# Performance work log

Measured on AMD Instinct MI355X. Metric: run time of the kernel, lower is better.

Reference implementation:

```python
import jax, jax.numpy as jnp
import numpy as np

INF = 1e10  # stand-in for the original global INF constant
D_MODEL = 1024
N_HEADS = 16
SCALE = float(np.sqrt(D_MODEL))  # Attention is built with full d_key, so scale = sqrt(d_model)


def setup_inputs() -> dict:
    key = jax.random.key(0)
    ks = jax.random.split(key, 8)
    B, S, D = 4, 2048, D_MODEL
    s = 1.0 / np.sqrt(D)
    return {
        "query": jax.random.normal(ks[0], (B, S, D), jnp.float32),
        "key": jax.random.normal(ks[1], (B, S, D), jnp.float32),
        "value": jax.random.normal(ks[2], (B, S, D), jnp.float32),
        "wq": jax.random.normal(ks[3], (D, D), jnp.float32) * s,
        "bq": jnp.zeros((D,), jnp.float32),
        "wk": jax.random.normal(ks[4], (D, D), jnp.float32) * s,
        "bk": jnp.zeros((D,), jnp.float32),
        "wv": jax.random.normal(ks[5], (D, D), jnp.float32) * s,
        "bv": jnp.zeros((D,), jnp.float32),
        "wo": jax.random.normal(ks[6], (D, D), jnp.float32) * s,
        "bo": jnp.zeros((D,), jnp.float32),
    }


def reference(query, key, value, wq, bq, wk, bk, wv, bv, wo, bo):
    B, S, D = query.shape
    H = N_HEADS
    dh = D // H
    q = query @ wq + bq
    k = key @ wk + bk
    v = value @ wv + bv
    # split heads: [B, S, H, dh]
    q = q.reshape(B, S, H, dh)
    k = k.reshape(B, S, H, dh)
    v = v.reshape(B, S, H, dh)
    # raw dot products (unscaled), then causal mask subtracted (as in original),
    # then divide by sqrt(d_key) and softmax
    scores = jnp.einsum("bqhd,bkhd->bhqk", q, k)
    causal = jnp.triu(jnp.ones((S, S), scores.dtype), k=1) * INF
    scores = scores - causal  # broadcast over [B, H]
    attn = jax.nn.softmax(scores / SCALE, axis=-1)
    out = jnp.einsum("bhqk,bkhd->bqhd", attn, v).reshape(B, S, D)
    return out @ wo + bo
```

## Files before the change

### kernel.cpp

```cpp
#include <hip/hip_runtime.h>
#include <hip/hip_bf16.h>

typedef __bf16 bf16_t;
typedef __bf16 bf16x8 __attribute__((ext_vector_type(8)));
typedef float f32x4 __attribute__((ext_vector_type(4)));

#define MFMA16(a, b, c) __builtin_amdgcn_mfma_f32_16x16x32_bf16((a), (b), (c), 0, 0, 0)

static constexpr int S_LEN = 2048;
static constexpr int DM = 1024;
static constexpr int NH = 16;
static constexpr int DH = 64;

struct WtArgs { const float* w[4]; bf16_t* o[4]; };

__global__ __launch_bounds__(256) void wt_kernel(WtArgs p) {
    int bid = blockIdx.x;
    int wi = bid >> 8;
    int tb = bid & 255;
    int k0 = (tb >> 4) * 64;
    int n0 = (tb & 15) * 64;
    const float* w = p.w[wi];
    bf16_t* o = p.o[wi];
    __shared__ bf16_t t[64 * 66];
    int tid = threadIdx.x;
#pragma unroll
    for (int i = 0; i < 4; ++i) {
        int f = tid + 256 * i;
        int row = f >> 4;
        int c4 = f & 15;
        f32x4 v = *reinterpret_cast<const f32x4*>(w + (size_t)(k0 + row) * DM + n0 + c4 * 4);
        int base = row * 66 + c4 * 4;
        t[base + 0] = (bf16_t)v[0];
        t[base + 1] = (bf16_t)v[1];
        t[base + 2] = (bf16_t)v[2];
        t[base + 3] = (bf16_t)v[3];
    }
    __syncthreads();
#pragma unroll
    for (int i = 0; i < 2; ++i) {
        int c = tid + 256 * i;
        int n = c >> 3;
        int ck = c & 7;
        union { bf16_t h[8]; uint4 u; } cv;
#pragma unroll
        for (int j = 0; j < 8; ++j) cv.h[j] = t[(ck * 8 + j) * 66 + n];
        *reinterpret_cast<uint4*>(o + (size_t)(n0 + n) * DM + k0 + ck * 8) = cv.u;
    }
}

template <int MODE>
__global__ __launch_bounds__(256) void gemm_k(const void* __restrict__ Ap,
                                              const bf16_t* __restrict__ BT,
                                              const float* __restrict__ bias,
                                              void* __restrict__ Cp, float alpha) {
    constexpr int K = 1024, N = 1024;
    int bid = blockIdx.x;
    int bm = bid >> 3, bn = bid & 7;
    int tid = threadIdx.x;
    int w = tid >> 6, l = tid & 63;
    int g = l >> 4, lc = l & 15;

    __shared__ bf16_t a_lds[128 * 40];
    __shared__ bf16_t b_lds[128 * 40];

    f32x4 zero = {0.f, 0.f, 0.f, 0.f};
    f32x4 acc[4][4];
#pragma unroll
    for (int m = 0; m < 4; ++m)
#pragma unroll
        for (int n = 0; n < 4; ++n) acc[m][n] = zero;

    int m0 = bm * 128, n0 = bn * 128;
    const float* Af = (const float*)Ap;
    const bf16_t* Ab = (const bf16_t*)Ap;
    int wr = (w >> 1) * 64, wc = (w & 1) * 64;

    for (int kt = 0; kt < K / 32; ++kt) {
        int k0 = kt * 32;
        __syncthreads();
        if constexpr (MODE != 1) {
#pragma unroll
            for (int i = 0; i < 4; ++i) {
                int f = tid + 256 * i;
                int row = f >> 3, c4 = f & 7;
                f32x4 v = *reinterpret_cast<const f32x4*>(Af + (size_t)(m0 + row) * K + k0 + c4 * 4);
                union { bf16_t h[4]; uint2 u; } cv;
                cv.h[0] = (bf16_t)v[0]; cv.h[1] = (bf16_t)v[1];
                cv.h[2] = (bf16_t)v[2]; cv.h[3] = (bf16_t)v[3];
                *reinterpret_cast<uint2*>(&a_lds[row * 40 + c4 * 4]) = cv.u;
            }
        } else {
#pragma unroll
            for (int i = 0; i < 2; ++i) {
                int c = tid + 256 * i;
                int row = c >> 2, ch = c & 3;
                uint4 v = *reinterpret_cast<const uint4*>(Ab + (size_t)(m0 + row) * K + k0 + ch * 8);
                *reinterpret_cast<uint4*>(&a_lds[row * 40 + ch * 8]) = v;
            }
        }
#pragma unroll
        for (int i = 0; i < 2; ++i) {
            int c = tid + 256 * i;
            int row = c >> 2, ch = c & 3;
            uint4 v = *reinterpret_cast<const uint4*>(BT + (size_t)(n0 + row) * K + k0 + ch * 8);
            *reinterpret_cast<uint4*>(&b_lds[row * 40 + ch * 8]) = v;
        }
        __syncthreads();

        bf16x8 af[4], bfr[4];
#pragma unroll
        for (int m = 0; m < 4; ++m)
            af[m] = *reinterpret_cast<bf16x8*>(&a_lds[(wr + m * 16 + lc) * 40 + g * 8]);
#pragma unroll
        for (int n = 0; n < 4; ++n)
            bfr[n] = *reinterpret_cast<bf16x8*>(&b_lds[(wc + n * 16 + lc) * 40 + g * 8]);
#pragma unroll
        for (int m = 0; m < 4; ++m)
#pragma unroll
            for (int n = 0; n < 4; ++n)
                acc[m][n] = MFMA16(af[m], bfr[n], acc[m][n]);
    }

#pragma unroll
    for (int n = 0; n < 4; ++n) {
        int ng = n0 + wc + n * 16 + lc;
        float bv = bias[ng];
#pragma unroll
        for (int m = 0; m < 4; ++m) {
#pragma unroll
            for (int r = 0; r < 4; ++r) {
                int mg = m0 + wr + m * 16 + g * 4 + r;
                float v = (acc[m][n][r] + bv) * alpha;
                if constexpr (MODE == 0) {
                    int b = mg >> 11, s = mg & 2047, h = ng >> 6, d = ng & 63;
                    ((bf16_t*)Cp)[(((size_t)(b * NH + h)) * S_LEN + s) * DH + d] = (bf16_t)v;
                } else if constexpr (MODE == 2) {
                    int b = mg >> 11, s = mg & 2047, h = ng >> 6, d = ng & 63;
                    ((bf16_t*)Cp)[(((size_t)(b * NH + h)) * DH + d) * S_LEN + s] = (bf16_t)v;
                } else {
                    ((float*)Cp)[(size_t)mg * N + ng] = v;
                }
            }
        }
    }
}

__global__ __launch_bounds__(256) void attn_kernel(const bf16_t* __restrict__ Qh,
                                                   const bf16_t* __restrict__ Kh,
                                                   const bf16_t* __restrict__ Vt,
                                                   bf16_t* __restrict__ AO) {
    int bid = blockIdx.x;
    int qt = 31 - (bid >> 6);
    int bh = bid & 63;
    int h = bh & 15;
    int b = bh >> 4;
    int tid = threadIdx.x;
    int w = tid >> 6, l = tid & 63;
    int g = l >> 4, lc = l & 15;
    int q0 = qt * 64 + w * 16;
    int q = q0 + lc;

    __shared__ bf16_t k_lds[64 * 80];
    __shared__ bf16_t v_lds[64 * 80];
    __shared__ bf16_t p_lds[4][16 * 80];

    size_t head_off = ((size_t)(b * NH + h)) * S_LEN * DH;
    const bf16_t* Kp = Kh + head_off;
    const bf16_t* Vp = Vt + head_off;

    bf16x8 qf[2];
    {
        const bf16_t* qp = Qh + head_off + (size_t)(q0 + lc) * DH + g * 8;
        qf[0] = *reinterpret_cast<const bf16x8*>(qp);
        qf[1] = *reinterpret_cast<const bf16x8*>(qp + 32);
    }

    f32x4 zero = {0.f, 0.f, 0.f, 0.f};
    f32x4 o_acc[4];
#pragma unroll
    for (int nt = 0; nt < 4; ++nt) o_acc[nt] = zero;
    float m_s = -1e30f, l_s = 0.f;

    int sw = lc & 7;

    for (int t = 0; t <= qt; ++t) {
        int kv0 = t * 64;
        __syncthreads();
#pragma unroll
        for (int i = 0; i < 2; ++i) {
            int c = tid + 256 * i;
            int row = c >> 3, ch = c & 7;
            uint4 v = *reinterpret_cast<const uint4*>(Kp + (size_t)(kv0 + row) * DH + ch * 8);
            *reinterpret_cast<uint4*>(&k_lds[row * 80 + (ch ^ (row & 7)) * 8]) = v;
        }
#pragma unroll
        for (int i = 0; i < 2; ++i) {
            int c = tid + 256 * i;
            int row = c >> 3, ch = c & 7;
            uint4 v = *reinterpret_cast<const uint4*>(Vp + (size_t)row * S_LEN + kv0 + ch * 8);
            *reinterpret_cast<uint4*>(&v_lds[row * 80 + (ch ^ (row & 7)) * 8]) = v;
        }
        __syncthreads();

        f32x4 sc[4];
#pragma unroll
        for (int nt = 0; nt < 4; ++nt) {
            int row = nt * 16 + lc;
            bf16x8 kf0 = *reinterpret_cast<bf16x8*>(&k_lds[row * 80 + ((g) ^ sw) * 8]);
            bf16x8 kf1 = *reinterpret_cast<bf16x8*>(&k_lds[row * 80 + ((4 + g) ^ sw) * 8]);
            f32x4 s = zero;
            s = MFMA16(kf0, qf[0], s);
            s = MFMA16(kf1, qf[1], s);
            sc[nt] = s;
        }
        if (t == qt) {
#pragma unroll
            for (int nt = 0; nt < 4; ++nt)
#pragma unroll
                for (int r = 0; r < 4; ++r) {
                    int kv = kv0 + nt * 16 + g * 4 + r;
                    if (kv > q) sc[nt][r] = -1e30f;
                }
        }
        float tm = sc[0][0];
#pragma unroll
        for (int nt = 0; nt < 4; ++nt)
#pragma unroll
            for (int r = 0; r < 4; ++r) tm = fmaxf(tm, sc[nt][r]);
        tm = fmaxf(tm, __shfl_xor(tm, 16, 64));
        tm = fmaxf(tm, __shfl_xor(tm, 32, 64));
        float mn = fmaxf(m_s, tm);
        float al = __expf(m_s - mn);
        m_s = mn;
#pragma unroll
        for (int nt = 0; nt < 4; ++nt)
#pragma unroll
            for (int r = 0; r < 4; ++r) sc[nt][r] = __expf(sc[nt][r] - m_s);
        float ts = 0.f;
#pragma unroll
        for (int nt = 0; nt < 4; ++nt)
            ts += sc[nt][0] + sc[nt][1] + sc[nt][2] + sc[nt][3];
        ts += __shfl_xor(ts, 16, 64);
        ts += __shfl_xor(ts, 32, 64);
        l_s = l_s * al + ts;
#pragma unroll
        for (int r = 0; r < 4; ++r) {
            float alr = __shfl(al, g * 4 + r, 64);
#pragma unroll
            for (int nt = 0; nt < 4; ++nt) o_acc[nt][r] *= alr;
        }
#pragma unroll
        for (int nt = 0; nt < 4; ++nt) {
            union { bf16_t hh[4]; uint2 u; } pk;
#pragma unroll
            for (int r = 0; r < 4; ++r) pk.hh[r] = (bf16_t)sc[nt][r];
            int cu = nt * 2 + (g >> 1);
            *reinterpret_cast<uint2*>(
                &p_lds[w][lc * 80 + (cu ^ sw) * 8 + (g & 1) * 4]) = pk.u;
        }
        bf16x8 pf0 = *reinterpret_cast<bf16x8*>(&p_lds[w][lc * 80 + ((g) ^ sw) * 8]);
        bf16x8 pf1 = *reinterpret_cast<bf16x8*>(&p_lds[w][lc * 80 + ((4 + g) ^ sw) * 8]);
#pragma unroll
        for (int nt = 0; nt < 4; ++nt) {
            int row = nt * 16 + lc;
            bf16x8 vf0 = *reinterpret_cast<bf16x8*>(&v_lds[row * 80 + ((g) ^ sw) * 8]);
            bf16x8 vf1 = *reinterpret_cast<bf16x8*>(&v_lds[row * 80 + ((4 + g) ^ sw) * 8]);
            o_acc[nt] = MFMA16(pf0, vf0, o_acc[nt]);
            o_acc[nt] = MFMA16(pf1, vf1, o_acc[nt]);
        }
    }

#pragma unroll
    for (int r = 0; r < 4; ++r) {
        float lr = __shfl(l_s, g * 4 + r, 64);
        float inv = 1.0f / lr;
        int qq = q0 + g * 4 + r;
        size_t base = ((size_t)b * S_LEN + qq) * DM + h * DH;
#pragma unroll
        for (int nt = 0; nt < 4; ++nt)
            AO[base + nt * 16 + lc] = (bf16_t)(o_acc[nt][r] * inv);
    }
}

extern "C" void kernel_launch(void* const* d_in, const int* in_sizes, int n_in,
                              void* d_out, int out_size, void* d_ws, size_t ws_size,
                              hipStream_t stream) {
    (void)in_sizes; (void)n_in; (void)out_size; (void)ws_size;
    const float* query = (const float*)d_in[0];
    const float* key   = (const float*)d_in[1];
    const float* value = (const float*)d_in[2];
    const float* wq = (const float*)d_in[3];
    const float* bq = (const float*)d_in[4];
    const float* wk = (const float*)d_in[5];
    const float* bk = (const float*)d_in[6];
    const float* wv = (const float*)d_in[7];
    const float* bv = (const float*)d_in[8];
    const float* wo = (const float*)d_in[9];
    const float* bo = (const float*)d_in[10];
    float* out = (float*)d_out;

    char* ws = (char*)d_ws;
    const size_t Mi = (size_t)1 << 20;
    bf16_t* wqT = (bf16_t*)(ws + 0 * Mi);
    bf16_t* wkT = (bf16_t*)(ws + 2 * Mi);
    bf16_t* wvT = (bf16_t*)(ws + 4 * Mi);
    bf16_t* woT = (bf16_t*)(ws + 6 * Mi);
    bf16_t* Qh  = (bf16_t*)(ws + 8 * Mi);
    bf16_t* Kh  = (bf16_t*)(ws + 24 * Mi);
    bf16_t* Vt  = (bf16_t*)(ws + 40 * Mi);
    bf16_t* AO  = (bf16_t*)(ws + 56 * Mi);

    WtArgs p;
    p.w[0] = wq; p.w[1] = wk; p.w[2] = wv; p.w[3] = wo;
    p.o[0] = wqT; p.o[1] = wkT; p.o[2] = wvT; p.o[3] = woT;
    wt_kernel<<<dim3(1024), dim3(256), 0, stream>>>(p);

    gemm_k<0><<<dim3(512), dim3(256), 0, stream>>>((const void*)query, wqT, bq, (void*)Qh, 0.03125f);
    gemm_k<0><<<dim3(512), dim3(256), 0, stream>>>((const void*)key,   wkT, bk, (void*)Kh, 1.0f);
    gemm_k<2><<<dim3(512), dim3(256), 0, stream>>>((const void*)value, wvT, bv, (void*)Vt, 1.0f);

    attn_kernel<<<dim3(2048), dim3(256), 0, stream>>>(Qh, Kh, Vt, AO);

    gemm_k<1><<<dim3(512), dim3(256), 0, stream>>>((const void*)AO, woT, bo, (void*)out, 1.0f);
}
```

Before: 251.4 us.

## Double-buffer GEMM and attention tiles with async global-to-LDS loads

Both the projection GEMM and the attention kernel now stage the next K or KV tile into a second LDS buffer using global_load_lds direct-to-LDS transfers while the current tile is consumed. This needs only one barrier per iteration instead of two and hides global load latency behind the MFMA work. The LDS row padding is dropped for the async-loaded tiles to match the direct-load layout, which may add bank conflicts on B-fragment reads. The transposed-V GEMM epilogue also packs four bf16 values into one vector store.

```diff
diff --git a/kernel.cpp b/kernel.cpp
--- a/kernel.cpp
+++ b/kernel.cpp
@@ -11,6 +11,12 @@
 static constexpr int DM = 1024;
 static constexpr int NH = 16;
 static constexpr int DH = 64;
+
+typedef const __attribute__((address_space(1))) unsigned int gu32;
+typedef __attribute__((address_space(3))) unsigned int lu32;
+__device__ __forceinline__ void gl_lds16(const void* src, void* dst) {
+    __builtin_amdgcn_global_load_lds((gu32*)src, (lu32*)dst, 16, 0, 0);
+}
 
 struct WtArgs { const float* w[4]; bf16_t* o[4]; };
 
@@ -55,14 +61,15 @@
                                               const float* __restrict__ bias,
                                               void* __restrict__ Cp, float alpha) {
     constexpr int K = 1024, N = 1024;
+    constexpr int AS = (MODE == 1) ? 32 : 40;
     int bid = blockIdx.x;
     int bm = bid >> 3, bn = bid & 7;
     int tid = threadIdx.x;
     int w = tid >> 6, l = tid & 63;
     int g = l >> 4, lc = l & 15;
 
-    __shared__ bf16_t a_lds[128 * 40];
-    __shared__ bf16_t b_lds[128 * 40];
+    __shared__ bf16_t a_buf[2][128 * AS];
+    __shared__ bf16_t b_buf[2][128 * 32];
 
     f32x4 zero = {0.f, 0.f, 0.f, 0.f};
     f32x4 acc[4][4];
@@ -76,9 +83,8 @@
     const bf16_t* Ab = (const bf16_t*)Ap;
     int wr = (w >> 1) * 64, wc = (w & 1) * 64;
 
-    for (int kt = 0; kt < K / 32; ++kt) {
+    auto stage = [&](int buf, int kt) {
         int k0 = kt * 32;
-        __syncthreads();
         if constexpr (MODE != 1) {
 #pragma unroll
             for (int i = 0; i < 4; ++i) {
@@ -88,58 +94,81 @@
                 union { bf16_t h[4]; uint2 u; } cv;
                 cv.h[0] = (bf16_t)v[0]; cv.h[1] = (bf16_t)v[1];
                 cv.h[2] = (bf16_t)v[2]; cv.h[3] = (bf16_t)v[3];
-                *reinterpret_cast<uint2*>(&a_lds[row * 40 + c4 * 4]) = cv.u;
+                *reinterpret_cast<uint2*>(&a_buf[buf][row * 40 + c4 * 4]) = cv.u;
             }
         } else {
 #pragma unroll
             for (int i = 0; i < 2; ++i) {
-                int c = tid + 256 * i;
-                int row = c >> 2, ch = c & 3;
-                uint4 v = *reinterpret_cast<const uint4*>(Ab + (size_t)(m0 + row) * K + k0 + ch * 8);
-                *reinterpret_cast<uint4*>(&a_lds[row * 40 + ch * 8]) = v;
+                int r16 = (w * 2 + i) * 16;
+                int row = r16 + (l >> 2), ch = l & 3;
+                gl_lds16(Ab + (size_t)(m0 + row) * K + k0 + ch * 8,
+                         &a_buf[buf][r16 * 32]);
             }
         }
 #pragma unroll
         for (int i = 0; i < 2; ++i) {
-            int c = tid + 256 * i;
-            int row = c >> 2, ch = c & 3;
-            uint4 v = *reinterpret_cast<const uint4*>(BT + (size_t)(n0 + row) * K + k0 + ch * 8);
-            *reinterpret_cast<uint4*>(&b_lds[row * 40 + ch * 8]) = v;
-        }
+            int r16 = (w * 2 + i) * 16;
+            int row = r16 + (l >> 2), ch = l & 3;
+            gl_lds16(BT + (size_t)(n0 + row) * K + k0 + ch * 8,
+                     &b_buf[buf][r16 * 32]);
+        }
+    };
+
+    stage(0, 0);
+    int cur = 0;
+    for (int kt = 0; kt < K / 32; ++kt) {
         __syncthreads();
-
+        if (kt + 1 < K / 32) stage(cur ^ 1, kt + 1);
         bf16x8 af[4], bfr[4];
 #pragma unroll
         for (int m = 0; m < 4; ++m)
-            af[m] = *reinterpret_cast<bf16x8*>(&a_lds[(wr + m * 16 + lc) * 40 + g * 8]);
+            af[m] = *reinterpret_cast<bf16x8*>(&a_buf[cur][(wr + m * 16 + lc) * AS + g * 8]);
 #pragma unroll
         for (int n = 0; n < 4; ++n)
-            bfr[n] = *reinterpret_cast<bf16x8*>(&b_lds[(wc + n * 16 + lc) * 40 + g * 8]);
+            bfr[n] = *reinterpret_cast<bf16x8*>(&b_buf[cur][(wc + n * 16 + lc) * 32 + g * 8]);
 #pragma unroll
         for (int m = 0; m < 4; ++m)
 #pragma unroll
             for (int n = 0; n < 4; ++n)
                 acc[m][n] = MFMA16(af[m], bfr[n], acc[m][n]);
-    }
-
-#pragma unroll
-    for (int n = 0; n < 4; ++n) {
-        int ng = n0 + wc + n * 16 + lc;
-        float bv = bias[ng];
-#pragma unroll
-        for (int m = 0; m < 4; ++m) {
-#pragma unroll
-            for (int r = 0; r < 4; ++r) {
-                int mg = m0 + wr + m * 16 + g * 4 + r;
-                float v = (acc[m][n][r] + bv) * alpha;
-                if constexpr (MODE == 0) {
-                    int b = mg >> 11, s = mg & 2047, h = ng >> 6, d = ng & 63;
-                    ((bf16_t*)Cp)[(((size_t)(b * NH + h)) * S_LEN + s) * DH + d] = (bf16_t)v;
-                } else if constexpr (MODE == 2) {
-                    int b = mg >> 11, s = mg & 2047, h = ng >> 6, d = ng & 63;
-                    ((bf16_t*)Cp)[(((size_t)(b * NH + h)) * DH + d) * S_LEN + s] = (bf16_t)v;
-                } else {
-                    ((float*)Cp)[(size_t)mg * N + ng] = v;
+        cur ^= 1;
+    }
+
+    if constexpr (MODE == 2) {
+#pragma unroll
+        for (int n = 0; n < 4; ++n) {
+            int ng = n0 + wc + n * 16 + lc;
+            float bv = bias[ng];
+            int h = ng >> 6, d = ng & 63;
+#pragma unroll
+            for (int m = 0; m < 4; ++m) {
+                int s0g = m0 + wr + m * 16 + g * 4;
+                int b = s0g >> 11, s0 = s0g & 2047;
+                union { bf16_t hh[4]; uint2 u; } pk;
+#pragma unroll
+                for (int r = 0; r < 4; ++r)
+                    pk.hh[r] = (bf16_t)((acc[m][n][r] + bv) * alpha);
+                *reinterpret_cast<uint2*>(
+                    &((bf16_t*)Cp)[(((size_t)(b * NH + h)) * DH + d) * S_LEN + s0]) = pk.u;
+            }
+        }
+    } else {
+#pragma unroll
+        for (int n = 0; n < 4; ++n) {
+            int ng = n0 + wc + n * 16 + lc;
+            float bv = bias[ng];
+#pragma unroll
+            for (int m = 0; m < 4; ++m) {
+#pragma unroll
+                for (int r = 0; r < 4; ++r) {
+                    int mg = m0 + wr + m * 16 + g * 4 + r;
+                    float v = (acc[m][n][r] + bv) * alpha;
+                    if constexpr (MODE == 0) {
+                        int b = mg >> 11, s = mg & 2047, h = ng >> 6, d = ng & 63;
+                        ((bf16_t*)Cp)[(((size_t)(b * NH + h)) * S_LEN + s) * DH + d] = (bf16_t)v;
+                    } else {
+                        ((float*)Cp)[(size_t)mg * N + ng] = v;
+                    }
                 }
             }
         }
@@ -161,9 +190,9 @@
     int q0 = qt * 64 + w * 16;
     int q = q0 + lc;
 
-    __shared__ bf16_t k_lds[64 * 80];
-    __shared__ bf16_t v_lds[64 * 80];
-    __shared__ bf16_t p_lds[4][16 * 80];
+    __shared__ bf16_t k_lds[2][64 * 64];
+    __shared__ bf16_t v_lds[2][64 * 64];
+    __shared__ bf16_t p_lds[4][16 * 64];
 
     size_t head_off = ((size_t)(b * NH + h)) * S_LEN * DH;
     const bf16_t* Kp = Kh + head_off;
@@ -184,31 +213,30 @@
 
     int sw = lc & 7;
 
+    auto stageKV = [&](int buf, int kv0) {
+#pragma unroll
+        for (int i = 0; i < 2; ++i) {
+            int r8 = w * 16 + i * 8;
+            int row = r8 + (l >> 3);
+            int sc_ = (l & 7) ^ (row & 7);
+            gl_lds16(Kp + (size_t)(kv0 + row) * DH + sc_ * 8, &k_lds[buf][r8 * 64]);
+            gl_lds16(Vp + (size_t)row * S_LEN + kv0 + sc_ * 8, &v_lds[buf][r8 * 64]);
+        }
+    };
+
+    stageKV(0, 0);
+    int cur = 0;
     for (int t = 0; t <= qt; ++t) {
         int kv0 = t * 64;
         __syncthreads();
-#pragma unroll
-        for (int i = 0; i < 2; ++i) {
-            int c = tid + 256 * i;
-            int row = c >> 3, ch = c & 7;
-            uint4 v = *reinterpret_cast<const uint4*>(Kp + (size_t)(kv0 + row) * DH + ch * 8);
-            *reinterpret_cast<uint4*>(&k_lds[row * 80 + (ch ^ (row & 7)) * 8]) = v;
-        }
-#pragma unroll
-        for (int i = 0; i < 2; ++i) {
-            int c = tid + 256 * i;
-            int row = c >> 3, ch = c & 7;
-            uint4 v = *reinterpret_cast<const uint4*>(Vp + (size_t)row * S_LEN + kv0 + ch * 8);
-            *reinterpret_cast<uint4*>(&v_lds[row * 80 + (ch ^ (row & 7)) * 8]) = v;
-        }
-        __syncthreads();
+        if (t < qt) stageKV(cur ^ 1, kv0 + 64);
 
         f32x4 sc[4];
 #pragma unroll
         for (int nt = 0; nt < 4; ++nt) {
             int row = nt * 16 + lc;
-            bf16x8 kf0 = *reinterpret_cast<bf16x8*>(&k_lds[row * 80 + ((g) ^ sw) * 8]);
-            bf16x8 kf1 = *reinterpret_cast<bf16x8*>(&k_lds[row * 80 + ((4 + g) ^ sw) * 8]);
+            bf16x8 kf0 = *reinterpret_cast<bf16x8*>(&k_lds[cur][row * 64 + ((g) ^ sw) * 8]);
+            bf16x8 kf1 = *reinterpret_cast<bf16x8*>(&k_lds[cur][row * 64 + ((4 + g) ^ sw) * 8]);
             f32x4 s = zero;
             s = MFMA16(kf0, qf[0], s);
             s = MFMA16(kf1, qf[1], s);
@@ -257,18 +285,19 @@
             for (int r = 0; r < 4; ++r) pk.hh[r] = (bf16_t)sc[nt][r];
             int cu = nt * 2 + (g >> 1);
             *reinterpret_cast<uint2*>(
-                &p_lds[w][lc * 80 + (cu ^ sw) * 8 + (g & 1) * 4]) = pk.u;
-        }
-        bf16x8 pf0 = *reinterpret_cast<bf16x8*>(&p_lds[w][lc * 80 + ((g) ^ sw) * 8]);
-        bf16x8 pf1 = *reinterpret_cast<bf16x8*>(&p_lds[w][lc * 80 + ((4 + g) ^ sw) * 8]);
+                &p_lds[w][lc * 64 + ((cu ^ sw) * 8) + (g & 1) * 4]) = pk.u;
+        }
+        bf16x8 pf0 = *reinterpret_cast<bf16x8*>(&p_lds[w][lc * 64 + ((g) ^ sw) * 8]);
+        bf16x8 pf1 = *reinterpret_cast<bf16x8*>(&p_lds[w][lc * 64 + ((4 + g) ^ sw) * 8]);
 #pragma unroll
         for (int nt = 0; nt < 4; ++nt) {
             int row = nt * 16 + lc;
-            bf16x8 vf0 = *reinterpret_cast<bf16x8*>(&v_lds[row * 80 + ((g) ^ sw) * 8]);
-            bf16x8 vf1 = *reinterpret_cast<bf16x8*>(&v_lds[row * 80 + ((4 + g) ^ sw) * 8]);
+            bf16x8 vf0 = *reinterpret_cast<bf16x8*>(&v_lds[cur][row * 64 + ((g) ^ sw) * 8]);
+            bf16x8 vf1 = *reinterpret_cast<bf16x8*>(&v_lds[cur][row * 64 + ((4 + g) ^ sw) * 8]);
             o_acc[nt] = MFMA16(pf0, vf0, o_acc[nt]);
             o_acc[nt] = MFMA16(pf1, vf1, o_acc[nt]);
         }
+        cur ^= 1;
     }
 
 #pragma unroll
```

Result: faster. 242.5 us (-3.5%).
